# Kernel tuning notes

Measured on AMD Instinct MI355X. Metric: run time of the kernel, lower is better.

Reference implementation:

```python
import jax, jax.numpy as jnp
import numpy as np

ALPHA = 0.2  # leaky relu negative slope
W_SIZE = 128  # window_size


def setup_inputs() -> dict:
    key = jax.random.key(0)
    ks = jax.random.split(key, 5)
    B, W, K, E = 4, 128, 256, 256  # E = 2*W (gatv2 doubles embed_dim)
    return {
        "x": jax.random.normal(ks[0], (B, W, K), dtype=jnp.float32),
        "lin_w": jax.random.normal(ks[1], (E, 2 * W), dtype=jnp.float32) * (1.0 / np.sqrt(2 * W)),
        "lin_b": jax.random.normal(ks[2], (E,), dtype=jnp.float32) * 0.02,
        "a_vec": jax.random.normal(ks[3], (E,), dtype=jnp.float32) * (1.414 / np.sqrt(E)),
        "bias": jax.random.normal(ks[4], (K, K), dtype=jnp.float32) * 0.02,
    }


def reference(x, lin_w, lin_b, a_vec, bias):
    # x: (B, W, K) -> v: (B, K, W), one W-length vector per node
    v = jnp.transpose(x, (0, 2, 1))
    # GATv2: lin(concat(v_i, v_j)) decomposed: concat @ lin_w.T = v_i @ W1.T + v_j @ W2.T
    W1 = lin_w[:, :W_SIZE]  # (E, W) applied to the repeated (source) block
    W2 = lin_w[:, W_SIZE:]  # (E, W) applied to the alternating (target) block
    u = jnp.einsum("bkw,ew->bke", v, W1)                 # (B, K, E)
    t = jnp.einsum("bkw,ew->bke", v, W2) + lin_b          # (B, K, E)
    pre = u[:, :, None, :] + t[:, None, :, :]             # (B, K, K, E) pairwise
    act = jax.nn.leaky_relu(pre, negative_slope=ALPHA)
    e = jnp.einsum("bije,e->bij", act, a_vec)             # (B, K, K)
    e = e + bias
    attn = jax.nn.softmax(e, axis=-1)
    h = jax.nn.sigmoid(jnp.einsum("bij,bjw->biw", attn, v))  # (B, K, W)
    return jnp.transpose(h, (0, 2, 1))  # (B, W, K)
```

## Files before the change

### kernel.cpp

```cpp
#include <hip/hip_runtime.h>
#include <math.h>

#define NB 4
#define WDIM 128
#define KDIM 256
#define EDIM 256

__device__ __forceinline__ float dot4(float4 a, float4 b) {
    return a.x * b.x + a.y * b.y + a.z * b.z + a.w * b.w;
}

__global__ __launch_bounds__(256) void k_ut8(const float* __restrict__ x,
                                             const float* __restrict__ lin_w,
                                             const float* __restrict__ lin_b,
                                             float* __restrict__ u_ws,
                                             float* __restrict__ tT_ws) {
    __shared__ float vrow[8 * WDIM];
    __shared__ float t_lds[64][9];
    const int blk = blockIdx.x;
    const int b  = blk >> 7;
    const int kt = (blk >> 2) & 31;
    const int eq = blk & 3;
    const int k0 = kt * 8;
    const int tid = threadIdx.x;
    const int el  = tid & 63;
    const int e   = eq * 64 + el;
    const int ks  = tid >> 6;

    if (tid < WDIM) {
        const float* xp = x + ((size_t)b * WDIM + tid) * KDIM + k0;
        float4 v0 = *(const float4*)xp;
        float4 v1 = *(const float4*)(xp + 4);
        vrow[0 * WDIM + tid] = v0.x; vrow[1 * WDIM + tid] = v0.y;
        vrow[2 * WDIM + tid] = v0.z; vrow[3 * WDIM + tid] = v0.w;
        vrow[4 * WDIM + tid] = v1.x; vrow[5 * WDIM + tid] = v1.y;
        vrow[6 * WDIM + tid] = v1.z; vrow[7 * WDIM + tid] = v1.w;
    }
    __syncthreads();

    const float4* wr = (const float4*)(lin_w + (size_t)e * 2 * WDIM);
    float u0 = 0.f, u1 = 0.f, t0 = 0.f, t1 = 0.f;
#pragma unroll 8
    for (int q = 0; q < 32; ++q) {
        float4 w1 = wr[q];
        float4 w2 = wr[32 + q];
        float4 va = *(const float4*)&vrow[(ks * 2 + 0) * WDIM + q * 4];
        float4 vb = *(const float4*)&vrow[(ks * 2 + 1) * WDIM + q * 4];
        u0 += dot4(w1, va); u1 += dot4(w1, vb);
        t0 += dot4(w2, va); t1 += dot4(w2, vb);
    }
    const float lb = lin_b[e];
    const int k = k0 + ks * 2;
    const size_t o0 = ((size_t)b * KDIM + k) * EDIM + e;
    u_ws[o0] = u0;  u_ws[o0 + EDIM] = u1;

    t_lds[el][ks * 2 + 0] = t0 + lb;
    t_lds[el][ks * 2 + 1] = t1 + lb;
    __syncthreads();

    const int e_w = tid >> 2;
    const int c2  = (tid & 3) * 2;
    float2 tv = make_float2(t_lds[e_w][c2], t_lds[e_w][c2 + 1]);
    *(float2*)(tT_ws + ((size_t)b * EDIM + eq * 64 + e_w) * KDIM + k0 + c2) = tv;
}

__global__ __launch_bounds__(1024, 1) void k_fused(const float* __restrict__ x,
                                                   const float* __restrict__ a_vec,
                                                   const float* __restrict__ bias,
                                                   const float* __restrict__ u_ws,
                                                   const float* __restrict__ tT_ws,
                                                   float* __restrict__ out) {
    __shared__ float z_lds[16][256];
    __shared__ float ru_lds[16];
    __shared__ float attn_lds[4][260];
    const int blk = blockIdx.x;
    const int b  = blk >> 6;
    const int it = blk & 63;
    const int i0 = it * 4;
    const int tid  = threadIdx.x;
    const int wv   = tid >> 6;
    const int lane = tid & 63;

    {
        const int i  = i0 + (wv >> 2);
        const int eq = wv & 3;
        const int e0 = eq * 64;
        const float* urow  = u_ws + ((size_t)b * KDIM + i) * EDIM + e0;
        const float* arow  = a_vec + e0;
        const float* tbase = tT_ws + ((size_t)b * EDIM + e0) * KDIM + lane * 4;

        float4 acc = make_float4(0.f, 0.f, 0.f, 0.f);
        float4 rt  = make_float4(0.f, 0.f, 0.f, 0.f);
        float ru = 0.f;
#pragma unroll 4
        for (int e4 = 0; e4 < 16; ++e4) {
            float4 uv = *(const float4*)(urow + e4 * 4);
            float4 av = *(const float4*)(arow + e4 * 4);
            float uc[4] = {uv.x, uv.y, uv.z, uv.w};
            float ac[4] = {av.x, av.y, av.z, av.w};
#pragma unroll
            for (int r = 0; r < 4; ++r) {
                float4 t4 = *(const float4*)(tbase + (size_t)(e4 * 4 + r) * KDIM);
                const float c = 0.4f * ac[r];
                const float d = 0.6f * ac[r];
                acc.x += c * fabsf(uc[r] + t4.x);  rt.x += d * t4.x;
                acc.y += c * fabsf(uc[r] + t4.y);  rt.y += d * t4.y;
                acc.z += c * fabsf(uc[r] + t4.z);  rt.z += d * t4.z;
                acc.w += c * fabsf(uc[r] + t4.w);  rt.w += d * t4.w;
                ru += d * uc[r];
            }
        }
        float4 z;
        z.x = acc.x + rt.x; z.y = acc.y + rt.y;
        z.z = acc.z + rt.z; z.w = acc.w + rt.w;
        *(float4*)&z_lds[wv][lane * 4] = z;
        if (lane == 0) ru_lds[wv] = ru;
    }
    __syncthreads();

    if (wv < 4) {
        float4 z0 = *(const float4*)&z_lds[wv * 4 + 0][lane * 4];
        float4 z1 = *(const float4*)&z_lds[wv * 4 + 1][lane * 4];
        float4 z2 = *(const float4*)&z_lds[wv * 4 + 2][lane * 4];
        float4 z3 = *(const float4*)&z_lds[wv * 4 + 3][lane * 4];
        const float ru = ru_lds[wv * 4] + ru_lds[wv * 4 + 1]
                       + ru_lds[wv * 4 + 2] + ru_lds[wv * 4 + 3];
        float4 bv = *(const float4*)(bias + (size_t)(i0 + wv) * KDIM + lane * 4);
        float4 ev;
        ev.x = z0.x + z1.x + z2.x + z3.x + ru + bv.x;
        ev.y = z0.y + z1.y + z2.y + z3.y + ru + bv.y;
        ev.z = z0.z + z1.z + z2.z + z3.z + ru + bv.z;
        ev.w = z0.w + z1.w + z2.w + z3.w + ru + bv.w;

        float m = fmaxf(fmaxf(ev.x, ev.y), fmaxf(ev.z, ev.w));
#pragma unroll
        for (int o = 1; o < 64; o <<= 1) m = fmaxf(m, __shfl_xor(m, o, 64));
        float4 p;
        p.x = __expf(ev.x - m); p.y = __expf(ev.y - m);
        p.z = __expf(ev.z - m); p.w = __expf(ev.w - m);
        float ssum = p.x + p.y + p.z + p.w;
#pragma unroll
        for (int o = 1; o < 64; o <<= 1) ssum += __shfl_xor(ssum, o, 64);
        const float inv = 1.0f / ssum;
        p.x *= inv; p.y *= inv; p.z *= inv; p.w *= inv;
        *(float4*)&attn_lds[wv][lane * 4] = p;
    }
    __syncthreads();

    const int s  = lane & 7;
    const int ww = lane >> 3;
    const int w  = wv * 8 + ww;
    const float* xr = x + ((size_t)b * WDIM + w) * KDIM;
    float acc[4] = {0.f, 0.f, 0.f, 0.f};
#pragma unroll
    for (int q = 0; q < 8; ++q) {
        float4 x4 = *(const float4*)(xr + q * 32 + s * 4);
#pragma unroll
        for (int ii = 0; ii < 4; ++ii) {
            float4 at = *(const float4*)&attn_lds[ii][q * 32 + s * 4];
            acc[ii] += dot4(at, x4);
        }
    }
#pragma unroll
    for (int ii = 0; ii < 4; ++ii) {
        acc[ii] += __shfl_xor(acc[ii], 1, 64);
        acc[ii] += __shfl_xor(acc[ii], 2, 64);
        acc[ii] += __shfl_xor(acc[ii], 4, 64);
    }
    if (s == 0) {
        float4 o;
        o.x = 1.f / (1.f + __expf(-acc[0]));
        o.y = 1.f / (1.f + __expf(-acc[1]));
        o.z = 1.f / (1.f + __expf(-acc[2]));
        o.w = 1.f / (1.f + __expf(-acc[3]));
        *(float4*)(out + ((size_t)b * WDIM + w) * KDIM + i0) = o;
    }
}

extern "C" void kernel_launch(void* const* d_in, const int* in_sizes, int n_in,
                              void* d_out, int out_size, void* d_ws, size_t ws_size,
                              hipStream_t stream) {
    (void)in_sizes; (void)n_in; (void)out_size; (void)ws_size;
    const float* x     = (const float*)d_in[0];
    const float* lin_w = (const float*)d_in[1];
    const float* lin_b = (const float*)d_in[2];
    const float* a_vec = (const float*)d_in[3];
    const float* bias  = (const float*)d_in[4];
    float* out = (float*)d_out;

    float* u_ws  = (float*)d_ws;
    float* tT_ws = u_ws + (size_t)NB * KDIM * EDIM;

    k_ut8<<<512, 256, 0, stream>>>(x, lin_w, lin_b, u_ws, tT_ws);
    k_fused<<<256, 1024, 0, stream>>>(x, a_vec, bias, u_ws, tT_ws, out);
}
```

Baseline: 39.16 us.

## Repartition fused attention kernel into 512 blocks of 256 threads, two rows each

The fused pairwise-score/softmax/aggregation kernel now handles 2 query rows per block with 4 waves instead of 4 rows with 16 waves. Each wave covers half of the embedding dimension, and the aggregation loops over 4 chunks of w. The block count doubles to 512, and smaller blocks with less LDS should let more blocks fit per CU and spread across more CUs than 256 blocks of 1024 threads. The cost is that the tT workspace and x rows are re-read by twice as many blocks, so L2 traffic rises.

Result: slower. 42.09 us (+7.5%).

```diff
diff --git a/kernel.cpp b/kernel.cpp
--- a/kernel.cpp
+++ b/kernel.cpp
@@ -10,11 +10,11 @@
     return a.x * b.x + a.y * b.y + a.z * b.z + a.w * b.w;
 }
 
-__global__ __launch_bounds__(256) void k_ut8(const float* __restrict__ x,
-                                             const float* __restrict__ lin_w,
-                                             const float* __restrict__ lin_b,
-                                             float* __restrict__ u_ws,
-                                             float* __restrict__ tT_ws) {
+__global__ __launch_bounds__(256) void k_ut10(const float* __restrict__ x,
+                                              const float* __restrict__ lin_w,
+                                              const float* __restrict__ lin_b,
+                                              float* __restrict__ u_ws,
+                                              float* __restrict__ tT_ws) {
     __shared__ float vrow[8 * WDIM];
     __shared__ float t_lds[64][9];
     const int blk = blockIdx.x;
@@ -64,27 +64,28 @@
     *(float2*)(tT_ws + ((size_t)b * EDIM + eq * 64 + e_w) * KDIM + k0 + c2) = tv;
 }
 
-__global__ __launch_bounds__(1024, 1) void k_fused(const float* __restrict__ x,
-                                                   const float* __restrict__ a_vec,
-                                                   const float* __restrict__ bias,
-                                                   const float* __restrict__ u_ws,
-                                                   const float* __restrict__ tT_ws,
-                                                   float* __restrict__ out) {
-    __shared__ float z_lds[16][256];
-    __shared__ float ru_lds[16];
-    __shared__ float attn_lds[4][260];
+__global__ __launch_bounds__(256) void k_fuse2(const float* __restrict__ x,
+                                               const float* __restrict__ a_vec,
+                                               const float* __restrict__ bias,
+                                               const float* __restrict__ u_ws,
+                                               const float* __restrict__ tT_ws,
+                                               float* __restrict__ out) {
+    __shared__ float z_lds[4][256];
+    __shared__ float ru_lds[4];
+    __shared__ float attn_lds[2][260];
     const int blk = blockIdx.x;
-    const int b  = blk >> 6;
-    const int it = blk & 63;
-    const int i0 = it * 4;
+    const int b  = blk >> 7;
+    const int ip = blk & 127;
+    const int i0 = ip * 2;
     const int tid  = threadIdx.x;
     const int wv   = tid >> 6;
     const int lane = tid & 63;
 
     {
-        const int i  = i0 + (wv >> 2);
-        const int eq = wv & 3;
-        const int e0 = eq * 64;
+        const int ii = wv >> 1;
+        const int eh = wv & 1;
+        const int i  = i0 + ii;
+        const int e0 = eh * 128;
         const float* urow  = u_ws + ((size_t)b * KDIM + i) * EDIM + e0;
         const float* arow  = a_vec + e0;
         const float* tbase = tT_ws + ((size_t)b * EDIM + e0) * KDIM + lane * 4;
@@ -93,7 +94,7 @@
         float4 rt  = make_float4(0.f, 0.f, 0.f, 0.f);
         float ru = 0.f;
 #pragma unroll 4
-        for (int e4 = 0; e4 < 16; ++e4) {
+        for (int e4 = 0; e4 < 32; ++e4) {
             float4 uv = *(const float4*)(urow + e4 * 4);
             float4 av = *(const float4*)(arow + e4 * 4);
             float uc[4] = {uv.x, uv.y, uv.z, uv.w};
@@ -118,19 +119,16 @@
     }
     __syncthreads();
 
-    if (wv < 4) {
-        float4 z0 = *(const float4*)&z_lds[wv * 4 + 0][lane * 4];
-        float4 z1 = *(const float4*)&z_lds[wv * 4 + 1][lane * 4];
-        float4 z2 = *(const float4*)&z_lds[wv * 4 + 2][lane * 4];
-        float4 z3 = *(const float4*)&z_lds[wv * 4 + 3][lane * 4];
-        const float ru = ru_lds[wv * 4] + ru_lds[wv * 4 + 1]
-                       + ru_lds[wv * 4 + 2] + ru_lds[wv * 4 + 3];
+    if (wv < 2) {
+        float4 z0 = *(const float4*)&z_lds[wv * 2 + 0][lane * 4];
+        float4 z1 = *(const float4*)&z_lds[wv * 2 + 1][lane * 4];
+        const float ru = ru_lds[wv * 2] + ru_lds[wv * 2 + 1];
         float4 bv = *(const float4*)(bias + (size_t)(i0 + wv) * KDIM + lane * 4);
         float4 ev;
-        ev.x = z0.x + z1.x + z2.x + z3.x + ru + bv.x;
-        ev.y = z0.y + z1.y + z2.y + z3.y + ru + bv.y;
-        ev.z = z0.z + z1.z + z2.z + z3.z + ru + bv.z;
-        ev.w = z0.w + z1.w + z2.w + z3.w + ru + bv.w;
+        ev.x = z0.x + z1.x + ru + bv.x;
+        ev.y = z0.y + z1.y + ru + bv.y;
+        ev.z = z0.z + z1.z + ru + bv.z;
+        ev.w = z0.w + z1.w + ru + bv.w;
 
         float m = fmaxf(fmaxf(ev.x, ev.y), fmaxf(ev.z, ev.w));
 #pragma unroll
@@ -149,31 +147,28 @@
 
     const int s  = lane & 7;
     const int ww = lane >> 3;
-    const int w  = wv * 8 + ww;
-    const float* xr = x + ((size_t)b * WDIM + w) * KDIM;
-    float acc[4] = {0.f, 0.f, 0.f, 0.f};
 #pragma unroll
-    for (int q = 0; q < 8; ++q) {
-        float4 x4 = *(const float4*)(xr + q * 32 + s * 4);
+    for (int c = 0; c < 4; ++c) {
+        const int w = wv * 32 + c * 8 + ww;
+        const float* xr = x + ((size_t)b * WDIM + w) * KDIM;
+        float acc0 = 0.f, acc1 = 0.f;
 #pragma unroll
-        for (int ii = 0; ii < 4; ++ii) {
-            float4 at = *(const float4*)&attn_lds[ii][q * 32 + s * 4];
-            acc[ii] += dot4(at, x4);
+        for (int q = 0; q < 8; ++q) {
+            float4 x4 = *(const float4*)(xr + q * 32 + s * 4);
+            float4 a0 = *(const float4*)&attn_lds[0][q * 32 + s * 4];
+            float4 a1 = *(const float4*)&attn_lds[1][q * 32 + s * 4];
+            acc0 += dot4(a0, x4);
+            acc1 += dot4(a1, x4);
         }
-    }
-#pragma unroll
-    for (int ii = 0; ii < 4; ++ii) {
-        acc[ii] += __shfl_xor(acc[ii], 1, 64);
-        acc[ii] += __shfl_xor(acc[ii], 2, 64);
-        acc[ii] += __shfl_xor(acc[ii], 4, 64);
-    }
-    if (s == 0) {
-        float4 o;
-        o.x = 1.f / (1.f + __expf(-acc[0]));
-        o.y = 1.f / (1.f + __expf(-acc[1]));
-        o.z = 1.f / (1.f + __expf(-acc[2]));
-        o.w = 1.f / (1.f + __expf(-acc[3]));
-        *(float4*)(out + ((size_t)b * WDIM + w) * KDIM + i0) = o;
+        acc0 += __shfl_xor(acc0, 1, 64); acc1 += __shfl_xor(acc1, 1, 64);
+        acc0 += __shfl_xor(acc0, 2, 64); acc1 += __shfl_xor(acc1, 2, 64);
+        acc0 += __shfl_xor(acc0, 4, 64); acc1 += __shfl_xor(acc1, 4, 64);
+        if (s == 0) {
+            float2 o2;
+            o2.x = 1.f / (1.f + __expf(-acc0));
+            o2.y = 1.f / (1.f + __expf(-acc1));
+            *(float2*)(out + ((size_t)b * WDIM + w) * KDIM + i0) = o2;
+        }
     }
 }
 
@@ -191,6 +186,6 @@
     float* u_ws  = (float*)d_ws;
     float* tT_ws = u_ws + (size_t)NB * KDIM * EDIM;
 
-    k_ut8<<<512, 256, 0, stream>>>(x, lin_w, lin_b, u_ws, tT_ws);
-    k_fused<<<256, 1024, 0, stream>>>(x, a_vec, bias, u_ws, tT_ws, out);
+    k_ut10<<<512, 256, 0, stream>>>(x, lin_w, lin_b, u_ws, tT_ws);
+    k_fuse2<<<512, 256, 0, stream>>>(x, a_vec, bias, u_ws, tT_ws, out);
 }
```
